# Kernel tuning notes

Hardware: AMD Instinct MI355X
Metric: run time of the kernel (lower is better)

Reference implementation:

```python
import jax, jax.numpy as jnp
import numpy as np

NEG = -1000000000.0
EPS = 1e-05

def setup_inputs() -> dict:
    key = jax.random.key(0)
    k1, k2, k3, k4, k5 = jax.random.split(key, 5)
    B, L, E, Q = 64, 2048, 512, 256
    encoded_vecs = jax.random.normal(k1, (B, L, E), dtype=jnp.float32)
    query = jax.random.normal(k2, (B, Q), dtype=jnp.float32)
    length = jax.random.randint(k3, (B,), 1, L + 1, dtype=jnp.int32)
    # Xavier-normal-ish params
    W1 = jax.random.normal(k4, (E + Q, E), dtype=jnp.float32) * jnp.sqrt(2.0 / (E + Q + E))
    b1 = jnp.zeros((E,), dtype=jnp.float32)
    v = jax.random.normal(k5, (E,), dtype=jnp.float32) * jnp.sqrt(2.0 / (E + 1))
    return {"encoded_vecs": encoded_vecs, "query": query, "length": length,
            "W1": W1, "b1": b1, "v": v}

def reference(encoded_vecs, query, length, W1, b1, v):
    B, L, E = encoded_vecs.shape
    # broadcast 2D query over the length dim (repeat in torch code)
    q = jnp.broadcast_to(query[:, None, :], (B, L, query.shape[-1]))
    h = jnp.concatenate([encoded_vecs, q], axis=2)            # [B, L, E+Q]
    u = jnp.tanh(jnp.einsum('blc,ce->ble', h, W1) + b1)       # [B, L, E]
    logits = jnp.einsum('ble,e->bl', u, v)                    # [B, L]
    # masked softmax (faithful to masked_softmax in source)
    mask = (jnp.arange(L)[None, :] < length[:, None])         # [B, L] bool
    masked_logits = jnp.where(mask, logits, NEG)
    max_logits = jnp.max(masked_logits, axis=1, keepdims=True)
    exps = jnp.exp(masked_logits - max_logits) * mask.astype(logits.dtype)
    attention = exps / (jnp.sum(exps, axis=1, keepdims=True) + EPS)  # [B, L]
    context = jnp.einsum('bl,ble->be', attention, encoded_vecs)      # [B, E]
    return (context, attention)
```

## Files before the change

kernel.cpp:

```cpp
#include <hip/hip_runtime.h>

typedef __attribute__((ext_vector_type(4))) float float4v;
typedef __attribute__((ext_vector_type(2))) float float2v;
typedef __attribute__((ext_vector_type(8))) short short8;
typedef __attribute__((ext_vector_type(4))) float f32x4;
typedef __attribute__((ext_vector_type(4))) int int4v;

#define NEGV (-1000000000.0f)

#define MTOT (64 * 2048)

__device__ __forceinline__ unsigned short f2bf(float f) {
    unsigned int u = __float_as_uint(f);
    u += 0x7fffu + ((u >> 16) & 1u);
    return (unsigned short)(u >> 16);
}

__device__ __forceinline__ void gload_lds16(const void* g, void* l) {
    __builtin_amdgcn_global_load_lds(
        (__attribute__((address_space(1))) unsigned int*)(unsigned long long)(g),
        (__attribute__((address_space(3))) unsigned int*)(unsigned int)(unsigned long long)(l),
        16, 0, 0);
}

__global__ __launch_bounds__(256)
void prep_wt_kernel(const float* __restrict__ W1, unsigned short* __restrict__ Wt) {
    __shared__ float t[32][33];
    int bx = blockIdx.x & 15;
    int by = blockIdx.x >> 4;
    int tx = threadIdx.x & 31;
    int ty = threadIdx.x >> 5;
    #pragma unroll
    for (int i = 0; i < 4; ++i)
        t[ty + 8 * i][tx] = W1[(bx * 32 + ty + 8 * i) * 512 + by * 32 + tx];
    __syncthreads();
    #pragma unroll
    for (int i = 0; i < 4; ++i)
        Wt[(by * 32 + ty + 8 * i) * 512 + bx * 32 + tx] = f2bf(t[tx][ty + 8 * i]);
}

__global__ void prep_qc_kernel(const float* __restrict__ query, const float* __restrict__ W1,
                               const float* __restrict__ b1, float* __restrict__ qc) {
    int b = blockIdx.x;
    int e = threadIdx.x;
    float acc0 = b1[e];
    float acc1 = b1[e + 256];
    const float* w = W1 + 512 * 512;
    for (int q = 0; q < 256; ++q) {
        float qv = query[b * 256 + q];
        acc0 += qv * w[q * 512 + e];
        acc1 += qv * w[q * 512 + e + 256];
    }
    qc[b * 512 + e] = acc0;
    qc[b * 512 + e + 256] = acc1;
}

__global__ __launch_bounds__(256)
void gemm_logits_kernel(const float* __restrict__ A,
                        const unsigned short* __restrict__ Wt,
                        const float* __restrict__ qc,
                        const float* __restrict__ v,
                        const int* __restrict__ length,
                        float* __restrict__ part)
{
    int bid = blockIdx.x;
    int x = bid & 7;
    int j = bid >> 3;
    int bm = (j >> 2) * 8 + x;
    int bn = j & 3;
    int b = bm >> 4;
    int l0 = (bm & 15) * 128;
    if (l0 >= length[b]) return;

    __shared__ float As[3 * 128 * 32];
    __shared__ unsigned short Bs[3 * 128 * 32];

    int tid = threadIdx.x;
    int lane = tid & 63;
    int w = tid >> 6;
    int wm = w >> 1, wn = w & 1;
    long row0 = (long)bm * 128;
    int col0 = bn * 128;

    const char* gA[4];
    const char* gB[2];
    #pragma unroll
    for (int i = 0; i < 4; ++i) {
        int off = (w * 4 + i) * 1024 + lane * 16;
        int r = off >> 7;
        int kbg = (off & 127) ^ ((r & 7) << 4);
        gA[i] = (const char*)A + (row0 + r) * 2048 + kbg;
    }
    #pragma unroll
    for (int i = 0; i < 2; ++i) {
        int off = (w * 2 + i) * 1024 + lane * 16;
        int r = off >> 6;
        int kbg = (off & 63) ^ (((r >> 1) & 3) << 4);
        gB[i] = (const char*)Wt + (long)(col0 + r) * 1024 + kbg;
    }

    int aoff[4][2], boff[4];
    int kb0 = 32 * (lane >> 4);
    #pragma unroll
    for (int mi = 0; mi < 4; ++mi) {
        int ar = wm * 64 + (lane & 15) + mi * 16;
        int swz = (ar & 7) << 4;
        aoff[mi][0] = ar * 128 + (kb0 ^ swz);
        aoff[mi][1] = ar * 128 + ((kb0 + 16) ^ swz);
    }
    int kbB = 16 * (lane >> 4);
    #pragma unroll
    for (int ni = 0; ni < 4; ++ni) {
        int br = wn * 64 + (lane & 15) + ni * 16;
        boff[ni] = br * 64 + (kbB ^ (((br >> 1) & 3) << 4));
    }

    f32x4 acc[4][4] = {};

    auto STAGE = [&](int t, char* la, char* lb) {
        gload_lds16(gA[0] + t * 128, la + w * 4096);
        gload_lds16(gA[1] + t * 128, la + w * 4096 + 1024);
        gload_lds16(gA[2] + t * 128, la + w * 4096 + 2048);
        gload_lds16(gA[3] + t * 128, la + w * 4096 + 3072);
        gload_lds16(gB[0] + t * 64, lb + w * 2048);
        gload_lds16(gB[1] + t * 64, lb + w * 2048 + 1024);
    };
    auto COMPUTE = [&](const char* as, const char* bs) {
        short8 af[4], bf[4];
        #pragma unroll
        for (int mi = 0; mi < 4; ++mi) {
            float4v xv = *(const float4v*)(as + aoff[mi][0]);
            float4v yv = *(const float4v*)(as + aoff[mi][1]);
            union { int4v i; short8 s; } u;
            asm("v_cvt_pk_bf16_f32 %0, %1, %2" : "=v"(u.i.x) : "v"(xv[0]), "v"(xv[1]));
            asm("v_cvt_pk_bf16_f32 %0, %1, %2" : "=v"(u.i.y) : "v"(xv[2]), "v"(xv[3]));
            asm("v_cvt_pk_bf16_f32 %0, %1, %2" : "=v"(u.i.z) : "v"(yv[0]), "v"(yv[1]));
            asm("v_cvt_pk_bf16_f32 %0, %1, %2" : "=v"(u.i.w) : "v"(yv[2]), "v"(yv[3]));
            af[mi] = u.s;
        }
        #pragma unroll
        for (int ni = 0; ni < 4; ++ni)
            bf[ni] = *(const short8*)(bs + boff[ni]);
        #pragma unroll
        for (int mi = 0; mi < 4; ++mi)
            #pragma unroll
            for (int ni = 0; ni < 4; ++ni)
                acc[mi][ni] = __builtin_amdgcn_mfma_f32_16x16x32_bf16(af[mi], bf[ni], acc[mi][ni], 0, 0, 0);
    };

    char* Ab = (char*)As;
    char* Bb = (char*)Bs;

    STAGE(0, Ab, Bb);
    STAGE(1, Ab + 16384, Bb + 8192);

    int cur = 0;
    #pragma unroll 1
    for (int t = 0; t < 15; ++t) {
        asm volatile("s_waitcnt vmcnt(6)" ::: "memory");
        __builtin_amdgcn_s_barrier();
        asm volatile("" ::: "memory");
        if (t < 14) {
            int tgt = cur == 0 ? 2 : cur - 1;
            STAGE(t + 2, Ab + tgt * 16384, Bb + tgt * 8192);
        }
        COMPUTE(Ab + cur * 16384, Bb + cur * 8192);
        cur = cur == 2 ? 0 : cur + 1;
    }
    asm volatile("s_waitcnt vmcnt(0)" ::: "memory");
    __builtin_amdgcn_s_barrier();
    asm volatile("" ::: "memory");
    COMPUTE(Ab + cur * 16384, Bb + cur * 8192);

    const float* qcb = qc + b * 512;
    float vcol[4], qcol[4];
    #pragma unroll
    for (int ni = 0; ni < 4; ++ni) {
        int c = col0 + wn * 64 + ni * 16 + (lane & 15);
        vcol[ni] = v[c];
        qcol[ni] = qcb[c];
    }
    float* pslice = part + (bn * 2 + wn) * MTOT + row0;
    int rbase = wm * 64 + 4 * (lane >> 4);
    #pragma unroll
    for (int mi = 0; mi < 4; ++mi) {
        #pragma unroll
        for (int j2 = 0; j2 < 4; ++j2) {
            float s = 0.f;
            #pragma unroll
            for (int ni = 0; ni < 4; ++ni) {
                float xx = acc[mi][ni][j2] + qcol[ni];
                float e2 = __expf(2.0f * xx);
                float tt = 1.0f - 2.0f * __builtin_amdgcn_rcpf(e2 + 1.0f);
                s += tt * vcol[ni];
            }
            s += __shfl_xor(s, 1);
            s += __shfl_xor(s, 2);
            s += __shfl_xor(s, 4);
            s += __shfl_xor(s, 8);
            if ((lane & 15) == 0)
                pslice[rbase + mi * 16 + j2] = s;
        }
    }
}

__global__ void softmax_kernel(const float* __restrict__ part, const int* __restrict__ length,
                               float* __restrict__ att, float* __restrict__ ctx) {
    int b = blockIdx.x;
    int len = length[b];
    int tid = threadIdx.x;
    int lane = tid & 63, wv = tid >> 6;
    const float* p0 = part + b * 2048;
    float* ab = att + b * 2048;

    ctx[b * 512 + tid] = 0.f;
    ctx[b * 512 + 256 + tid] = 0.f;

    float vals[8];
    float mymax = -3.402823466e38f;
    #pragma unroll
    for (int i = 0; i < 8; ++i) {
        int l = tid + i * 256;
        float xv = NEGV;
        if (l < len) {
            xv = 0.f;
            #pragma unroll
            for (int s = 0; s < 8; ++s)
                xv += p0[s * MTOT + l];
        }
        vals[i] = xv;
        mymax = fmaxf(mymax, xv);
    }
    #pragma unroll
    for (int m = 32; m; m >>= 1) mymax = fmaxf(mymax, __shfl_xor(mymax, m));
    __shared__ float sm[4];
    if (lane == 0) sm[wv] = mymax;
    __syncthreads();
    float bmax = fmaxf(fmaxf(sm[0], sm[1]), fmaxf(sm[2], sm[3]));

    float mysum = 0.f;
    #pragma unroll
    for (int i = 0; i < 8; ++i) {
        int l = tid + i * 256;
        float e = (l < len) ? __expf(vals[i] - bmax) : 0.f;
        vals[i] = e;
        mysum += e;
    }
    #pragma unroll
    for (int m = 32; m; m >>= 1) mysum += __shfl_xor(mysum, m);
    __shared__ float ss[4];
    if (lane == 0) ss[wv] = mysum;
    __syncthreads();
    float tot = ss[0] + ss[1] + ss[2] + ss[3];
    float inv = 1.0f / (tot + 1e-5f);
    #pragma unroll
    for (int i = 0; i < 8; ++i) {
        int l = tid + i * 256;
        ab[l] = vals[i] * inv;
    }
}

__global__ void ctx_kernel(const float* __restrict__ att, const float* __restrict__ enc,
                           const int* __restrict__ length, float* __restrict__ ctx) {
    int b = blockIdx.x;
    int lc = blockIdx.y;
    int len = length[b];
    int l0 = lc * 128;
    if (l0 >= len) return;
    int lim = len - l0;
    if (lim > 128) lim = 128;

    int t = threadIdx.x;
    const float* ab = att + b * 2048 + l0;
    const float* eb = enc + ((long)(b * 2048 + l0)) * 512 + t * 2;
    float c0 = 0.f, c1 = 0.f;
    #pragma unroll 4
    for (int l = 0; l < lim; ++l) {
        float a = ab[l];
        float2v e = *(const float2v*)(eb);
        eb += 512;
        c0 += a * e.x;
        c1 += a * e.y;
    }
    atomicAdd(&ctx[b * 512 + 2 * t], c0);
    atomicAdd(&ctx[b * 512 + 2 * t + 1], c1);
}

extern "C" void kernel_launch(void* const* d_in, const int* in_sizes, int n_in,
                              void* d_out, int out_size, void* d_ws, size_t ws_size,
                              hipStream_t stream) {
    const float* enc    = (const float*)d_in[0];
    const float* query  = (const float*)d_in[1];
    const int*   length = (const int*)d_in[2];
    const float* W1     = (const float*)d_in[3];
    const float* b1     = (const float*)d_in[4];
    const float* v      = (const float*)d_in[5];

    float* out = (float*)d_out;
    float* ctx = out;
    float* att = out + 64 * 512;

    char* ws = (char*)d_ws;
    float* part        = (float*)ws;
    float* qc          = (float*)(ws + 8 * MTOT * 4);
    unsigned short* Wt = (unsigned short*)(ws + 8 * MTOT * 4 + 64 * 512 * 4);

    prep_wt_kernel<<<256, 256, 0, stream>>>(W1, Wt);
    prep_qc_kernel<<<64, 256, 0, stream>>>(query, W1, b1, qc);

    gemm_logits_kernel<<<4096, 256, 0, stream>>>(enc, Wt, qc, v, length, part);

    softmax_kernel<<<64, 256, 0, stream>>>(part, length, att, ctx);

    dim3 g3(64, 16);
    ctx_kernel<<<g3, 256, 0, stream>>>(att, enc, length, ctx);
}
```

Before: 152.2 us.

## Convert A tile to bf16 once in registers before LDS, restructure GEMM pipeline

The GEMM mainloop now loads fp32 A tiles into registers, converts them to bf16 once and writes them to a half-size bf16 LDS buffer. Previously the fp32 tile sat in LDS and every wave re-converted it at MFMA-operand time. This is meant to cut LDS footprint, LDS read bandwidth and redundant conversions, and it pairs with a fully unrolled register-double-buffered pipeline and a launch-bounds occupancy hint of 3 blocks. The cost is higher register pressure, extra LDS writes, and a global-to-register latency that has to be hidden by the software pipeline. The qc prep loop is also unrolled by 8.

```diff
diff --git a/kernel.cpp b/kernel.cpp
--- a/kernel.cpp
+++ b/kernel.cpp
@@ -46,6 +46,7 @@
     float acc0 = b1[e];
     float acc1 = b1[e + 256];
     const float* w = W1 + 512 * 512;
+    #pragma unroll 8
     for (int q = 0; q < 256; ++q) {
         float qv = query[b * 256 + q];
         acc0 += qv * w[q * 512 + e];
@@ -55,7 +56,7 @@
     qc[b * 512 + e + 256] = acc1;
 }
 
-__global__ __launch_bounds__(256)
+__global__ __launch_bounds__(256, 3)
 void gemm_logits_kernel(const float* __restrict__ A,
                         const unsigned short* __restrict__ Wt,
                         const float* __restrict__ qc,
@@ -72,7 +73,7 @@
     int l0 = (bm & 15) * 128;
     if (l0 >= length[b]) return;
 
-    __shared__ float As[3 * 128 * 32];
+    __shared__ unsigned short As[3 * 128 * 32];
     __shared__ unsigned short Bs[3 * 128 * 32];
 
     int tid = threadIdx.x;
@@ -82,95 +83,115 @@
     long row0 = (long)bm * 128;
     int col0 = bn * 128;
 
-    const char* gA[4];
-    const char* gB[2];
-    #pragma unroll
-    for (int i = 0; i < 4; ++i) {
-        int off = (w * 4 + i) * 1024 + lane * 16;
-        int r = off >> 7;
-        int kbg = (off & 127) ^ ((r & 7) << 4);
-        gA[i] = (const char*)A + (row0 + r) * 2048 + kbg;
-    }
-    #pragma unroll
-    for (int i = 0; i < 2; ++i) {
-        int off = (w * 2 + i) * 1024 + lane * 16;
+    int ar_r = w * 32 + (lane >> 1);
+    int ar_h = lane & 1;
+    const char* gAr = (const char*)A + (row0 + ar_r) * 2048 + ar_h * 64;
+    int asw = ((ar_r >> 1) & 3) << 4;
+    int awr0 = ar_r * 64 + ((ar_h * 32) ^ asw);
+    int awr1 = ar_r * 64 + ((ar_h * 32 + 16) ^ asw);
+
+    const char* gB0;
+    const char* gB1;
+    {
+        int off = (w * 2 + 0) * 1024 + lane * 16;
         int r = off >> 6;
-        int kbg = (off & 63) ^ (((r >> 1) & 3) << 4);
-        gB[i] = (const char*)Wt + (long)(col0 + r) * 1024 + kbg;
-    }
-
-    int aoff[4][2], boff[4];
-    int kb0 = 32 * (lane >> 4);
+        gB0 = (const char*)Wt + (long)(col0 + r) * 1024 + ((off & 63) ^ (((r >> 1) & 3) << 4));
+        off = (w * 2 + 1) * 1024 + lane * 16;
+        r = off >> 6;
+        gB1 = (const char*)Wt + (long)(col0 + r) * 1024 + ((off & 63) ^ (((r >> 1) & 3) << 4));
+    }
+
+    int aoff[4], boff[4];
+    int kb = 16 * (lane >> 4);
     #pragma unroll
     for (int mi = 0; mi < 4; ++mi) {
         int ar = wm * 64 + (lane & 15) + mi * 16;
-        int swz = (ar & 7) << 4;
-        aoff[mi][0] = ar * 128 + (kb0 ^ swz);
-        aoff[mi][1] = ar * 128 + ((kb0 + 16) ^ swz);
-    }
-    int kbB = 16 * (lane >> 4);
+        aoff[mi] = ar * 64 + (kb ^ (((ar >> 1) & 3) << 4));
+    }
     #pragma unroll
     for (int ni = 0; ni < 4; ++ni) {
         int br = wn * 64 + (lane & 15) + ni * 16;
-        boff[ni] = br * 64 + (kbB ^ (((br >> 1) & 3) << 4));
+        boff[ni] = br * 64 + (kb ^ (((br >> 1) & 3) << 4));
     }
 
     f32x4 acc[4][4] = {};
-
-    auto STAGE = [&](int t, char* la, char* lb) {
-        gload_lds16(gA[0] + t * 128, la + w * 4096);
-        gload_lds16(gA[1] + t * 128, la + w * 4096 + 1024);
-        gload_lds16(gA[2] + t * 128, la + w * 4096 + 2048);
-        gload_lds16(gA[3] + t * 128, la + w * 4096 + 3072);
-        gload_lds16(gB[0] + t * 64, lb + w * 2048);
-        gload_lds16(gB[1] + t * 64, lb + w * 2048 + 1024);
-    };
-    auto COMPUTE = [&](const char* as, const char* bs) {
-        short8 af[4], bf[4];
-        #pragma unroll
-        for (int mi = 0; mi < 4; ++mi) {
-            float4v xv = *(const float4v*)(as + aoff[mi][0]);
-            float4v yv = *(const float4v*)(as + aoff[mi][1]);
-            union { int4v i; short8 s; } u;
-            asm("v_cvt_pk_bf16_f32 %0, %1, %2" : "=v"(u.i.x) : "v"(xv[0]), "v"(xv[1]));
-            asm("v_cvt_pk_bf16_f32 %0, %1, %2" : "=v"(u.i.y) : "v"(xv[2]), "v"(xv[3]));
-            asm("v_cvt_pk_bf16_f32 %0, %1, %2" : "=v"(u.i.z) : "v"(yv[0]), "v"(yv[1]));
-            asm("v_cvt_pk_bf16_f32 %0, %1, %2" : "=v"(u.i.w) : "v"(yv[2]), "v"(yv[3]));
-            af[mi] = u.s;
-        }
-        #pragma unroll
-        for (int ni = 0; ni < 4; ++ni)
-            bf[ni] = *(const short8*)(bs + boff[ni]);
-        #pragma unroll
-        for (int mi = 0; mi < 4; ++mi)
-            #pragma unroll
-            for (int ni = 0; ni < 4; ++ni)
-                acc[mi][ni] = __builtin_amdgcn_mfma_f32_16x16x32_bf16(af[mi], bf[ni], acc[mi][ni], 0, 0, 0);
-    };
-
-    char* Ab = (char*)As;
-    char* Bb = (char*)Bs;
-
-    STAGE(0, Ab, Bb);
-    STAGE(1, Ab + 16384, Bb + 8192);
-
-    int cur = 0;
-    #pragma unroll 1
-    for (int t = 0; t < 15; ++t) {
-        asm volatile("s_waitcnt vmcnt(6)" ::: "memory");
-        __builtin_amdgcn_s_barrier();
-        asm volatile("" ::: "memory");
-        if (t < 14) {
-            int tgt = cur == 0 ? 2 : cur - 1;
-            STAGE(t + 2, Ab + tgt * 16384, Bb + tgt * 8192);
-        }
-        COMPUTE(Ab + cur * 16384, Bb + cur * 8192);
-        cur = cur == 2 ? 0 : cur + 1;
-    }
-    asm volatile("s_waitcnt vmcnt(0)" ::: "memory");
+    float4v P0, P1, P2, P3, Q0, Q1, Q2, Q3;
+
+#define GISSUE(t, R0, R1, R2, R3, sI) do {                                   \
+    const char* ga_ = gAr + (t) * 128;                                       \
+    R0 = *(const float4v*)(ga_);                                             \
+    R1 = *(const float4v*)(ga_ + 16);                                        \
+    R2 = *(const float4v*)(ga_ + 32);                                        \
+    R3 = *(const float4v*)(ga_ + 48);                                        \
+    char* lb_ = (char*)Bs + (sI) * 8192 + w * 2048;                          \
+    gload_lds16(gB0 + (t) * 64, lb_);                                        \
+    gload_lds16(gB1 + (t) * 64, lb_ + 1024);                                 \
+} while (0)
+
+#define CVTW(R0, R1, R2, R3, sW) do {                                        \
+    union { int4v i; short8 s; } u0_, u1_;                                   \
+    asm("v_cvt_pk_bf16_f32 %0, %1, %2" : "=v"(u0_.i.x) : "v"(R0[0]), "v"(R0[1])); \
+    asm("v_cvt_pk_bf16_f32 %0, %1, %2" : "=v"(u0_.i.y) : "v"(R0[2]), "v"(R0[3])); \
+    asm("v_cvt_pk_bf16_f32 %0, %1, %2" : "=v"(u0_.i.z) : "v"(R1[0]), "v"(R1[1])); \
+    asm("v_cvt_pk_bf16_f32 %0, %1, %2" : "=v"(u0_.i.w) : "v"(R1[2]), "v"(R1[3])); \
+    asm("v_cvt_pk_bf16_f32 %0, %1, %2" : "=v"(u1_.i.x) : "v"(R2[0]), "v"(R2[1])); \
+    asm("v_cvt_pk_bf16_f32 %0, %1, %2" : "=v"(u1_.i.y) : "v"(R2[2]), "v"(R2[3])); \
+    asm("v_cvt_pk_bf16_f32 %0, %1, %2" : "=v"(u1_.i.z) : "v"(R3[0]), "v"(R3[1])); \
+    asm("v_cvt_pk_bf16_f32 %0, %1, %2" : "=v"(u1_.i.w) : "v"(R3[2]), "v"(R3[3])); \
+    char* aw_ = (char*)As + (sW) * 8192;                                     \
+    *(short8*)(aw_ + awr0) = u0_.s;                                          \
+    *(short8*)(aw_ + awr1) = u1_.s;                                          \
+} while (0)
+
+#define KCOMP(sC) do {                                                       \
+    const char* as_ = (const char*)As + (sC) * 8192;                         \
+    const char* bs_ = (const char*)Bs + (sC) * 8192;                         \
+    short8 af_[4], bf_[4];                                                   \
+    _Pragma("unroll")                                                        \
+    for (int mi = 0; mi < 4; ++mi) af_[mi] = *(const short8*)(as_ + aoff[mi]); \
+    _Pragma("unroll")                                                        \
+    for (int ni = 0; ni < 4; ++ni) bf_[ni] = *(const short8*)(bs_ + boff[ni]); \
+    _Pragma("unroll")                                                        \
+    for (int mi = 0; mi < 4; ++mi)                                           \
+        _Pragma("unroll")                                                    \
+        for (int ni = 0; ni < 4; ++ni)                                       \
+            acc[mi][ni] = __builtin_amdgcn_mfma_f32_16x16x32_bf16(af_[mi], bf_[ni], acc[mi][ni], 0, 0, 0); \
+} while (0)
+
+#define KITER(t, L0, L1, L2, L3, C0, C1, C2, C3, sC, sW, sI, ISS, VM) do {   \
+    if (ISS) GISSUE((t) + 2, L0, L1, L2, L3, sI);                            \
+    KCOMP(sC);                                                               \
+    asm volatile("s_waitcnt vmcnt(" #VM ")" ::: "memory");                   \
+    CVTW(C0, C1, C2, C3, sW);                                                \
+    asm volatile("s_waitcnt lgkmcnt(0)" ::: "memory");                       \
+    __builtin_amdgcn_s_barrier();                                            \
+    asm volatile("" ::: "memory");                                           \
+} while (0)
+
+    GISSUE(0, P0, P1, P2, P3, 0);
+    GISSUE(1, Q0, Q1, Q2, Q3, 1);
+    asm volatile("s_waitcnt vmcnt(6)" ::: "memory");
+    CVTW(P0, P1, P2, P3, 0);
+    asm volatile("s_waitcnt lgkmcnt(0)" ::: "memory");
     __builtin_amdgcn_s_barrier();
     asm volatile("" ::: "memory");
-    COMPUTE(Ab + cur * 16384, Bb + cur * 8192);
+
+    KITER(0,  P0,P1,P2,P3, Q0,Q1,Q2,Q3, 0,1,2, 1, 6);
+    KITER(1,  Q0,Q1,Q2,Q3, P0,P1,P2,P3, 1,2,0, 1, 6);
+    KITER(2,  P0,P1,P2,P3, Q0,Q1,Q2,Q3, 2,0,1, 1, 6);
+    KITER(3,  Q0,Q1,Q2,Q3, P0,P1,P2,P3, 0,1,2, 1, 6);
+    KITER(4,  P0,P1,P2,P3, Q0,Q1,Q2,Q3, 1,2,0, 1, 6);
+    KITER(5,  Q0,Q1,Q2,Q3, P0,P1,P2,P3, 2,0,1, 1, 6);
+    KITER(6,  P0,P1,P2,P3, Q0,Q1,Q2,Q3, 0,1,2, 1, 6);
+    KITER(7,  Q0,Q1,Q2,Q3, P0,P1,P2,P3, 1,2,0, 1, 6);
+    KITER(8,  P0,P1,P2,P3, Q0,Q1,Q2,Q3, 2,0,1, 1, 6);
+    KITER(9,  Q0,Q1,Q2,Q3, P0,P1,P2,P3, 0,1,2, 1, 6);
+    KITER(10, P0,P1,P2,P3, Q0,Q1,Q2,Q3, 1,2,0, 1, 6);
+    KITER(11, Q0,Q1,Q2,Q3, P0,P1,P2,P3, 2,0,1, 1, 6);
+    KITER(12, P0,P1,P2,P3, Q0,Q1,Q2,Q3, 0,1,2, 1, 6);
+    KITER(13, Q0,Q1,Q2,Q3, P0,P1,P2,P3, 1,2,0, 1, 6);
+    KITER(14, P0,P1,P2,P3, Q0,Q1,Q2,Q3, 2,0,1, 0, 0);
+    KCOMP(0);
 
     const float* qcb = qc + b * 512;
     float vcol[4], qcol[4];
```

Result: faster. 145.0 us (-4.7%).

## Replace LDS-pipelined GEMM with direct global-load MFMA tiles of 64 rows

Applied to the files above, without the earlier changes.

Drops the triple-buffered global_load_lds staging and swizzled LDS layout in the logits GEMM. Each wave now loads its A and W fragments straight from global memory into registers, with 64-row by 64-column tiles per wave and 8 column groups across two blocks. The inline v_cvt_pk_bf16_f32 conversion is replaced with software rounding, and the query-projection loop is unrolled. This removes LDS traffic and barriers, but adds redundant global reads across waves, exposes load latency because there is no software pipelining, and adds more ALU work for the bf16 conversion.

```diff
diff --git a/kernel.cpp b/kernel.cpp
--- a/kernel.cpp
+++ b/kernel.cpp
@@ -4,7 +4,6 @@
 typedef __attribute__((ext_vector_type(2))) float float2v;
 typedef __attribute__((ext_vector_type(8))) short short8;
 typedef __attribute__((ext_vector_type(4))) float f32x4;
-typedef __attribute__((ext_vector_type(4))) int int4v;
 
 #define NEGV (-1000000000.0f)
 
@@ -14,13 +13,6 @@
     unsigned int u = __float_as_uint(f);
     u += 0x7fffu + ((u >> 16) & 1u);
     return (unsigned short)(u >> 16);
-}
-
-__device__ __forceinline__ void gload_lds16(const void* g, void* l) {
-    __builtin_amdgcn_global_load_lds(
-        (__attribute__((address_space(1))) unsigned int*)(unsigned long long)(g),
-        (__attribute__((address_space(3))) unsigned int*)(unsigned int)(unsigned long long)(l),
-        16, 0, 0);
 }
 
 __global__ __launch_bounds__(256)
@@ -46,6 +38,7 @@
     float acc0 = b1[e];
     float acc1 = b1[e + 256];
     const float* w = W1 + 512 * 512;
+    #pragma unroll 8
     for (int q = 0; q < 256; ++q) {
         float qv = query[b * 256 + q];
         acc0 += qv * w[q * 512 + e];
@@ -66,122 +59,56 @@
     int bid = blockIdx.x;
     int x = bid & 7;
     int j = bid >> 3;
-    int bm = (j >> 2) * 8 + x;
-    int bn = j & 3;
-    int b = bm >> 4;
-    int l0 = (bm & 15) * 128;
+    int p = (j >> 1) * 8 + x;
+    int h = j & 1;
+    int b = p >> 5;
+    int l0 = (p & 31) * 64;
     if (l0 >= length[b]) return;
 
-    __shared__ float As[3 * 128 * 32];
-    __shared__ unsigned short Bs[3 * 128 * 32];
-
-    int tid = threadIdx.x;
-    int lane = tid & 63;
-    int w = tid >> 6;
-    int wm = w >> 1, wn = w & 1;
-    long row0 = (long)bm * 128;
-    int col0 = bn * 128;
-
-    const char* gA[4];
-    const char* gB[2];
-    #pragma unroll
-    for (int i = 0; i < 4; ++i) {
-        int off = (w * 4 + i) * 1024 + lane * 16;
-        int r = off >> 7;
-        int kbg = (off & 127) ^ ((r & 7) << 4);
-        gA[i] = (const char*)A + (row0 + r) * 2048 + kbg;
-    }
-    #pragma unroll
-    for (int i = 0; i < 2; ++i) {
-        int off = (w * 2 + i) * 1024 + lane * 16;
-        int r = off >> 6;
-        int kbg = (off & 63) ^ (((r >> 1) & 3) << 4);
-        gB[i] = (const char*)Wt + (long)(col0 + r) * 1024 + kbg;
-    }
-
-    int aoff[4][2], boff[4];
-    int kb0 = 32 * (lane >> 4);
-    #pragma unroll
-    for (int mi = 0; mi < 4; ++mi) {
-        int ar = wm * 64 + (lane & 15) + mi * 16;
-        int swz = (ar & 7) << 4;
-        aoff[mi][0] = ar * 128 + (kb0 ^ swz);
-        aoff[mi][1] = ar * 128 + ((kb0 + 16) ^ swz);
-    }
-    int kbB = 16 * (lane >> 4);
-    #pragma unroll
-    for (int ni = 0; ni < 4; ++ni) {
-        int br = wn * 64 + (lane & 15) + ni * 16;
-        boff[ni] = br * 64 + (kbB ^ (((br >> 1) & 3) << 4));
-    }
+    int lane = threadIdx.x & 63;
+    int w = threadIdx.x >> 6;
+    int cg = h * 4 + w;
+    long row0 = (long)p * 64;
+    int col0 = cg * 64;
+
+    const float* Abase = A + (row0 + (lane & 15)) * 512 + (lane >> 4) * 8;
+    const unsigned short* Bbase = Wt + (long)(col0 + (lane & 15)) * 512 + (lane >> 4) * 8;
 
     f32x4 acc[4][4] = {};
 
-    auto STAGE = [&](int t, char* la, char* lb) {
-        gload_lds16(gA[0] + t * 128, la + w * 4096);
-        gload_lds16(gA[1] + t * 128, la + w * 4096 + 1024);
-        gload_lds16(gA[2] + t * 128, la + w * 4096 + 2048);
-        gload_lds16(gA[3] + t * 128, la + w * 4096 + 3072);
-        gload_lds16(gB[0] + t * 64, lb + w * 2048);
-        gload_lds16(gB[1] + t * 64, lb + w * 2048 + 1024);
-    };
-    auto COMPUTE = [&](const char* as, const char* bs) {
+    for (int k0 = 0; k0 < 512; k0 += 32) {
         short8 af[4], bf[4];
         #pragma unroll
         for (int mi = 0; mi < 4; ++mi) {
-            float4v xv = *(const float4v*)(as + aoff[mi][0]);
-            float4v yv = *(const float4v*)(as + aoff[mi][1]);
-            union { int4v i; short8 s; } u;
-            asm("v_cvt_pk_bf16_f32 %0, %1, %2" : "=v"(u.i.x) : "v"(xv[0]), "v"(xv[1]));
-            asm("v_cvt_pk_bf16_f32 %0, %1, %2" : "=v"(u.i.y) : "v"(xv[2]), "v"(xv[3]));
-            asm("v_cvt_pk_bf16_f32 %0, %1, %2" : "=v"(u.i.z) : "v"(yv[0]), "v"(yv[1]));
-            asm("v_cvt_pk_bf16_f32 %0, %1, %2" : "=v"(u.i.w) : "v"(yv[2]), "v"(yv[3]));
-            af[mi] = u.s;
+            const float* ap = Abase + mi * 16 * 512 + k0;
+            float4v x0 = *(const float4v*)(ap);
+            float4v x1 = *(const float4v*)(ap + 4);
+            union { unsigned int u[4]; short8 s; } pk;
+            pk.u[0] = (unsigned int)f2bf(x0[0]) | ((unsigned int)f2bf(x0[1]) << 16);
+            pk.u[1] = (unsigned int)f2bf(x0[2]) | ((unsigned int)f2bf(x0[3]) << 16);
+            pk.u[2] = (unsigned int)f2bf(x1[0]) | ((unsigned int)f2bf(x1[1]) << 16);
+            pk.u[3] = (unsigned int)f2bf(x1[2]) | ((unsigned int)f2bf(x1[3]) << 16);
+            af[mi] = pk.s;
         }
         #pragma unroll
         for (int ni = 0; ni < 4; ++ni)
-            bf[ni] = *(const short8*)(bs + boff[ni]);
+            bf[ni] = *(const short8*)(Bbase + ni * 16 * 512 + k0);
         #pragma unroll
         for (int mi = 0; mi < 4; ++mi)
             #pragma unroll
             for (int ni = 0; ni < 4; ++ni)
                 acc[mi][ni] = __builtin_amdgcn_mfma_f32_16x16x32_bf16(af[mi], bf[ni], acc[mi][ni], 0, 0, 0);
-    };
-
-    char* Ab = (char*)As;
-    char* Bb = (char*)Bs;
-
-    STAGE(0, Ab, Bb);
-    STAGE(1, Ab + 16384, Bb + 8192);
-
-    int cur = 0;
-    #pragma unroll 1
-    for (int t = 0; t < 15; ++t) {
-        asm volatile("s_waitcnt vmcnt(6)" ::: "memory");
-        __builtin_amdgcn_s_barrier();
-        asm volatile("" ::: "memory");
-        if (t < 14) {
-            int tgt = cur == 0 ? 2 : cur - 1;
-            STAGE(t + 2, Ab + tgt * 16384, Bb + tgt * 8192);
-        }
-        COMPUTE(Ab + cur * 16384, Bb + cur * 8192);
-        cur = cur == 2 ? 0 : cur + 1;
-    }
-    asm volatile("s_waitcnt vmcnt(0)" ::: "memory");
-    __builtin_amdgcn_s_barrier();
-    asm volatile("" ::: "memory");
-    COMPUTE(Ab + cur * 16384, Bb + cur * 8192);
+    }
 
     const float* qcb = qc + b * 512;
     float vcol[4], qcol[4];
     #pragma unroll
     for (int ni = 0; ni < 4; ++ni) {
-        int c = col0 + wn * 64 + ni * 16 + (lane & 15);
+        int c = col0 + ni * 16 + (lane & 15);
         vcol[ni] = v[c];
         qcol[ni] = qcb[c];
     }
-    float* pslice = part + (bn * 2 + wn) * MTOT + row0;
-    int rbase = wm * 64 + 4 * (lane >> 4);
+    float* pslice = part + cg * MTOT + row0;
     #pragma unroll
     for (int mi = 0; mi < 4; ++mi) {
         #pragma unroll
@@ -199,7 +126,7 @@
             s += __shfl_xor(s, 4);
             s += __shfl_xor(s, 8);
             if ((lane & 15) == 0)
-                pslice[rbase + mi * 16 + j2] = s;
+                pslice[mi * 16 + 4 * (lane >> 4) + j2] = s;
         }
     }
 }
```

After: 327.6 us. +115.2%, slower.
